# Kernel tuning notes

Measured on AMD Instinct MI355X. Metric: run time of the kernel, lower is better.

Reference implementation:

```python
import jax, jax.numpy as jnp
import numpy as np

VAR0, VAR1 = 0.1, 0.2   # cfg['variance']
THRESH = 0.5            # overlap_thresh
THETA = 0.01
NEGPOS = 3


def decode(loc, priors):
    # priors center-form [P,4]; returns point-form boxes [P,4]
    cxcy = priors[:, :2] + loc[:, :2] * VAR0 * priors[:, 2:]
    wh = priors[:, 2:] * jnp.exp(loc[:, 2:] * VAR1)
    return jnp.concatenate([cxcy - wh * 0.5, cxcy + wh * 0.5], axis=1)


def center_size(b):
    return jnp.concatenate([(b[:, :2] + b[:, 2:]) * 0.5, b[:, 2:] - b[:, :2]], axis=1)


def encode(matched, priors_c):
    # matched point-form [P,4], priors_c center-form [P,4]
    g_cxcy = ((matched[:, :2] + matched[:, 2:]) * 0.5 - priors_c[:, :2]) / (VAR0 * priors_c[:, 2:])
    g_wh = jnp.log((matched[:, 2:] - matched[:, :2]) / priors_c[:, 2:]) / VAR1
    return jnp.concatenate([g_cxcy, g_wh], axis=1)


def jaccard(a, b):
    # a [G,4], b [P,4] point form -> IoU [G,P]
    lt = jnp.maximum(a[:, None, :2], b[None, :, :2])
    rb = jnp.minimum(a[:, None, 2:], b[None, :, 2:])
    wh = jnp.clip(rb - lt, 0.0)
    inter = wh[..., 0] * wh[..., 1]
    area_a = ((a[:, 2] - a[:, 0]) * (a[:, 3] - a[:, 1]))[:, None]
    area_b = ((b[:, 2] - b[:, 0]) * (b[:, 3] - b[:, 1]))[None, :]
    return inter / (area_a + area_b - inter)


def _match_one(truths, labels, gt_mask, arm_loc, priors):
    # refine_match with arm_loc (use_ARM=True path)
    P = priors.shape[0]
    G = truths.shape[0]
    dec = decode(arm_loc, priors)                                 # [P,4]
    ov = jnp.where(gt_mask[:, None], jaccard(truths, dec), -1.0)  # [G,P], padded GT masked out
    best_prior_idx = jnp.argmax(ov, axis=1)                       # [G]
    best_truth_ov = jnp.max(ov, axis=0)                           # [P]
    best_truth_idx = jnp.argmax(ov, axis=0)                       # [P]
    safe = jnp.where(gt_mask, best_prior_idx, P)                  # OOB index -> dropped scatter
    best_truth_ov = best_truth_ov.at[safe].set(2.0, mode='drop')  # force-match each valid GT
    best_truth_idx = best_truth_idx.at[safe].set(jnp.arange(G), mode='drop')
    matched = truths[best_truth_idx]                              # [P,4]
    conf = jnp.where(best_truth_ov < THRESH, 0, labels[best_truth_idx])
    loc = encode(matched, center_size(dec))
    return loc, conf


def forward(arm_loc, arm_conf, odm_loc, odm_conf, priors, targets, num_gts):
    B, P, C = odm_conf.shape
    truths = targets[..., :4]
    labels = targets[..., 4].astype(jnp.int32)
    gt_mask = jnp.arange(targets.shape[1])[None, :] < num_gts[:, None]
    loc_t, conf_t = jax.vmap(_match_one, in_axes=(0, 0, 0, 0, None))(
        truths, labels, gt_mask,
        jax.lax.stop_gradient(arm_loc), jax.lax.stop_gradient(priors))
    loc_t = jax.lax.stop_gradient(loc_t)    # loc_t.requires_grad = False
    conf_t = jax.lax.stop_gradient(conf_t)

    # ARM objectness filter on positives
    p_obj = jax.nn.softmax(arm_conf, axis=2)[:, :, 1]
    pos = (conf_t > 0) & (p_obj > THETA)

    # masked smooth-L1 localization loss (sum)
    posf = pos[..., None].astype(odm_loc.dtype)
    d = jnp.abs(odm_loc * posf - loc_t * posf)
    loss_l = jnp.sum(jnp.where(d < 1.0, 0.5 * d * d, d - 0.5))

    # hard negative mining on per-prior softmax loss
    batch_conf = odm_conf.reshape(-1, C)
    lc = jax.nn.logsumexp(batch_conf, axis=1) - jnp.take_along_axis(
        batch_conf, conf_t.reshape(-1, 1), axis=1)[:, 0]
    lc = jnp.where(pos.reshape(-1), 0.0, lc).reshape(B, P)
    loss_idx = jnp.argsort(-lc, axis=1)
    idx_rank = jnp.argsort(loss_idx, axis=1)
    num_pos = jnp.sum(pos.astype(jnp.int32), axis=1, keepdims=True)  # [B,1]
    num_neg = jnp.minimum(NEGPOS * num_pos, P - 1)
    neg = idx_rank < num_neg
    mask = pos | neg

    # masked cross entropy (compute on zeroed-out logits like the original, then mask)
    conf_p = (odm_conf * mask[..., None].astype(odm_conf.dtype)).reshape(-1, C)
    tgt = jnp.where(mask, conf_t, 0).reshape(-1)
    logp = jax.nn.log_softmax(conf_p, axis=1)
    ce = -jnp.take_along_axis(logp, tgt[:, None], axis=1)[:, 0]
    loss_c = jnp.sum(ce * mask.reshape(-1).astype(ce.dtype))

    N = jnp.sum(num_pos).astype(jnp.float32)
    return loss_l / N, loss_c / N


def setup_inputs():
    key = jax.random.key(0)
    ks = jax.random.split(key, 10)
    B, P, C, G = 32, 16320, 21, 40
    arm_loc = jax.random.normal(ks[0], (B, P, 4), jnp.float32) * 0.1
    arm_conf = jax.random.normal(ks[1], (B, P, 2), jnp.float32)
    odm_loc = jax.random.normal(ks[2], (B, P, 4), jnp.float32) * 0.1
    odm_conf = jax.random.normal(ks[3], (B, P, C), jnp.float32)
    # priors in center form with positive sizes
    pc = jax.random.uniform(ks[4], (P, 2), jnp.float32, 0.1, 0.9)
    pwh = jax.random.uniform(ks[5], (P, 2), jnp.float32, 0.05, 0.3)
    priors = jnp.concatenate([pc, pwh], axis=1)
    # GT boxes in point form with positive area, labels in 1..C-1, padded to G=40
    gc = jax.random.uniform(ks[6], (B, G, 2), jnp.float32, 0.2, 0.8)
    gwh = jax.random.uniform(ks[7], (B, G, 2), jnp.float32, 0.05, 0.3)
    boxes = jnp.concatenate([gc - gwh * 0.5, gc + gwh * 0.5], axis=-1)
    labels = jax.random.randint(ks[8], (B, G, 1), 1, C).astype(jnp.float32)
    targets = jnp.concatenate([boxes, labels], axis=-1)
    num_gts = jax.random.randint(ks[9], (B,), 1, G + 1).astype(jnp.int32)
    return {"arm_loc": arm_loc, "arm_conf": arm_conf, "odm_loc": odm_loc,
            "odm_conf": odm_conf, "priors": priors, "targets": targets,
            "num_gts": num_gts}


def reference(arm_loc, arm_conf, odm_loc, odm_conf, priors, targets, num_gts):
    return forward(arm_loc, arm_conf, odm_loc, odm_conf, priors, targets, num_gts)
```

## Files before the change

### kernel.cpp

```cpp
#include <hip/hip_runtime.h>
#include <math.h>

#define VAR0 0.1f
#define VAR1 0.2f
#define THRESH 0.5f
#define THETA 0.01f
#define MAXG 64
#define BLK 256
#define SELT 1024
#define NCH 16
#define NB 4096
#define CAP 2048

__device__ __forceinline__ float4 decode_box(float4 l, float4 pr) {
    float cx = pr.x + l.x * VAR0 * pr.z;
    float cy = pr.y + l.y * VAR0 * pr.w;
    float w = pr.z * expf(l.z * VAR1);
    float h = pr.w * expf(l.w * VAR1);
    return make_float4(cx - w * 0.5f, cy - h * 0.5f, cx + w * 0.5f, cy + h * 0.5f);
}

__device__ __forceinline__ unsigned wave_umax_bits(unsigned v) {
    int x = (int)v;
    int t;
    t = __builtin_amdgcn_update_dpp(0, x, 0x111, 0xf, 0xf, true);  x = (t > x) ? t : x;
    t = __builtin_amdgcn_update_dpp(0, x, 0x112, 0xf, 0xf, true);  x = (t > x) ? t : x;
    t = __builtin_amdgcn_update_dpp(0, x, 0x114, 0xf, 0xf, true);  x = (t > x) ? t : x;
    t = __builtin_amdgcn_update_dpp(0, x, 0x118, 0xf, 0xf, true);  x = (t > x) ? t : x;
    t = __builtin_amdgcn_update_dpp(0, x, 0x142, 0xa, 0xf, false); x = (t > x) ? t : x;
    t = __builtin_amdgcn_update_dpp(0, x, 0x143, 0xc, 0xf, false); x = (t > x) ? t : x;
    return (unsigned)__builtin_amdgcn_readlane(x, 63);
}

__global__ void k_iou(const float* __restrict__ arm_loc, const float* __restrict__ priors,
                      const float* __restrict__ targets, const int* __restrict__ num_gts,
                      unsigned long long* __restrict__ bt,
                      unsigned long long* __restrict__ bpw,
                      int B, int P, int G) {
    int b = blockIdx.y;
    int p = blockIdx.x * blockDim.x + threadIdx.x;
    int tid = threadIdx.x;
    int lane = tid & 63, wid = tid >> 6;
    int wavebase = blockIdx.x * (int)blockDim.x + (tid & ~63);
    __shared__ float4 st4[MAXG];
    __shared__ float  stl[MAXG];
    __shared__ unsigned long long wk[4][MAXG];
    __shared__ int sng;
    if (tid == 0) sng = num_gts[b];
    for (int i = tid; i < G * 4; i += blockDim.x) {
        int g = i >> 2, k = i & 3;
        ((float*)&st4[g])[k] = targets[(size_t)b * G * 5 + g * 5 + k];
    }
    for (int g = tid; g < G; g += blockDim.x) stl[g] = targets[(size_t)b * G * 5 + g * 5 + 4];
    __syncthreads();
    int ng = sng;
    bool ok = p < P;
    float4 d = make_float4(0.f, 0.f, 0.f, 0.f);
    float areaB = 0.f;
    size_t i = (size_t)b * P + (ok ? p : 0);
    if (ok) {
        float4 l = ((const float4*)arm_loc)[i];
        float4 pr = ((const float4*)priors)[p];
        d = decode_box(l, pr);
        areaB = (d.z - d.x) * (d.w - d.y);
    }
    float bov = -2.0f; int bidx = 0;
    for (int g = 0; g < ng; ++g) {
        float4 t = st4[g];
        unsigned vbits = 0u;
        if (ok) {
            float lt0 = fmaxf(t.x, d.x), lt1 = fmaxf(t.y, d.y);
            float rb0 = fminf(t.z, d.z), rb1 = fminf(t.w, d.w);
            float w = rb0 - lt0; if (w < 0.f) w = 0.f;
            float h = rb1 - lt1; if (h < 0.f) h = 0.f;
            float inter = w * h;
            float areaA = (t.z - t.x) * (t.w - t.y);
            float ov = inter / (areaA + areaB - inter);
            if (ov > bov) { bov = ov; bidx = g; }
            vbits = __float_as_uint(ov);
        }
        unsigned om = wave_umax_bits(vbits);
        unsigned long long mask = __ballot(vbits == om);
        if (lane == 0) {
            int p_win = wavebase + (int)__builtin_ctzll(mask);
            wk[wid][g] = ((unsigned long long)om << 32)
                       | (unsigned long long)(0xFFFFFFFFu - (unsigned)p_win);
        }
    }
    if (ok)
        bt[i] = ((unsigned long long)__float_as_uint(bov) << 32) | (unsigned)bidx;
    __syncthreads();
    if (tid < ng) {
        unsigned long long k0 = wk[0][tid], k1 = wk[1][tid];
        unsigned long long k2 = wk[2][tid], k3 = wk[3][tid];
        unsigned long long m01 = k0 > k1 ? k0 : k1;
        unsigned long long m23 = k2 > k3 ? k2 : k3;
        unsigned long long m = m01 > m23 ? m01 : m23;
        bpw[(size_t)(b * G + tid) * gridDim.x + blockIdx.x] = m;
    }
}

__global__ void k_fix(const int* __restrict__ num_gts, const unsigned long long* __restrict__ bpw,
                      unsigned long long* __restrict__ bt, int B, int P, int G, int NBX) {
    int g = blockIdx.x, b = blockIdx.y;
    int lane = threadIdx.x;
    if (g >= num_gts[b]) return;
    const unsigned long long* src = bpw + (size_t)(b * G + g) * NBX;
    unsigned long long key = 0ull;
    for (int j = lane; j < NBX; j += 64) {
        unsigned long long v = src[j];
        if (v > key) key = v;
    }
    for (int off = 32; off > 0; off >>= 1) {
        unsigned long long o = __shfl_down(key, (unsigned)off, 64);
        if (o > key) key = o;
    }
    if (lane == 0) {
        unsigned p = 0xFFFFFFFFu - (unsigned)(key & 0xFFFFFFFFull);
        unsigned long long fkey = ((unsigned long long)0x40000000u << 32) | (unsigned)g;
        atomicMax(&bt[(size_t)b * P + p], fkey);
    }
}

__global__ void k_main(const float* __restrict__ arm_loc, const float* __restrict__ priors,
                       const float* __restrict__ arm_conf,
                       const float* __restrict__ odm_loc, const float* __restrict__ odm_conf,
                       const float* __restrict__ targets,
                       const unsigned long long* __restrict__ bt,
                       float* __restrict__ ce, unsigned char* __restrict__ posm,
                       float* __restrict__ partL, int* __restrict__ partN,
                       int B, int P, int C, int G) {
    int b = blockIdx.y;
    int p0 = blockIdx.x * BLK;
    int tid = threadIdx.x;
    int p = p0 + tid;
    __shared__ float4 st4[MAXG];
    __shared__ float  stl[MAXG];
    __shared__ float oc_s[BLK * 21];
    for (int i2 = tid; i2 < G * 4; i2 += BLK) {
        int g = i2 >> 2, k = i2 & 3;
        ((float*)&st4[g])[k] = targets[(size_t)b * G * 5 + g * 5 + k];
    }
    for (int g = tid; g < G; g += BLK) stl[g] = targets[(size_t)b * G * 5 + g * 5 + 4];
    int nrows = P - p0; if (nrows > BLK) nrows = BLK;
    int nf = nrows * C;
    const float* ocb = odm_conf + ((size_t)b * P + p0) * C;
    int nf4 = nf >> 2;
    const float4* ocb4 = (const float4*)ocb;
    for (int i2 = tid; i2 < nf4; i2 += BLK) ((float4*)oc_s)[i2] = ocb4[i2];
    if (tid < (nf & 3)) oc_s[(nf4 << 2) + tid] = ocb[(nf4 << 2) + tid];
    __syncthreads();
    float lsum = 0.f; int pc = 0;
    if (p < P) {
        size_t i = (size_t)b * P + p;
        unsigned long long mv = bt[i];
        float bov = __uint_as_float((unsigned)(mv >> 32));
        int bidx = (int)(mv & 0xFFFFFFFFull);
        int conf_t = (bov < THRESH) ? 0 : (int)stl[bidx];
        float2 c = ((const float2*)arm_conf)[i];
        float mm = fmaxf(c.x, c.y);
        float e0 = expf(c.x - mm), e1 = expf(c.y - mm);
        float p_obj = e1 / (e0 + e1);
        bool pos = (conf_t > 0) && (p_obj > THETA);
        if (pos) {
            pc = 1;
            float4 l = ((const float4*)arm_loc)[i];
            float4 pr = ((const float4*)priors)[p];
            float4 d = decode_box(l, pr);
            float pcx = (d.x + d.z) * 0.5f, pcy = (d.y + d.w) * 0.5f;
            float pw = d.z - d.x, ph = d.w - d.y;
            float4 t = st4[bidx];
            float g0 = ((t.x + t.z) * 0.5f - pcx) / (VAR0 * pw);
            float g1 = ((t.y + t.w) * 0.5f - pcy) / (VAR0 * ph);
            float g2 = logf((t.z - t.x) / pw) / VAR1;
            float g3 = logf((t.w - t.y) / ph) / VAR1;
            float4 ol = ((const float4*)odm_loc)[i];
            float dd;
            dd = fabsf(ol.x - g0); lsum += (dd < 1.f) ? 0.5f*dd*dd : dd - 0.5f;
            dd = fabsf(ol.y - g1); lsum += (dd < 1.f) ? 0.5f*dd*dd : dd - 0.5f;
            dd = fabsf(ol.z - g2); lsum += (dd < 1.f) ? 0.5f*dd*dd : dd - 0.5f;
            dd = fabsf(ol.w - g3); lsum += (dd < 1.f) ? 0.5f*dd*dd : dd - 0.5f;
        }
        const float* oc = oc_s + tid * C;
        float mx = oc[0];
        for (int j = 1; j < C; ++j) mx = fmaxf(mx, oc[j]);
        float sume = 0.f;
        for (int j = 0; j < C; ++j) sume += expf(oc[j] - mx);
        float lse = mx + logf(sume);
        float cev = lse - oc[conf_t];
        ce[i] = cev;
        posm[i] = pos ? 1 : 0;
    }
    __shared__ float rl[BLK];
    __shared__ int rc[BLK];
    rl[tid] = lsum; rc[tid] = pc;
    __syncthreads();
    for (int off = BLK/2; off > 0; off >>= 1) {
        if (tid < off) { rl[tid] += rl[tid+off]; rc[tid] += rc[tid+off]; }
        __syncthreads();
    }
    if (tid == 0) {
        partL[b * gridDim.x + blockIdx.x] = rl[0];
        partN[b * gridDim.x + blockIdx.x] = rc[0];
    }
}

__global__ __launch_bounds__(SELT) void k_select(
        const float* __restrict__ ce, const unsigned char* __restrict__ posm,
        const int* __restrict__ partN, int NBX,
        float* __restrict__ partC, int* __restrict__ npos, int P) {
    int b = blockIdx.x;
    int tid = threadIdx.x;
    int lane = tid & 63, wid = tid >> 6;
    __shared__ unsigned hist[NB];
    __shared__ float cv[CAP];
    __shared__ int   ci[CAP];
    __shared__ int   sums[SELT];
    __shared__ int   redi[16];
    __shared__ float redf[16];
    __shared__ int sh_base[16];
    __shared__ int sh_m, sh_b1, sh_k1, sh_npos, sh_istar, sh_kk, sh_cum;
    __shared__ unsigned sh_T, sh_pref;
    __shared__ float sh_mx;

    int c0 = 0;
    for (int j = tid; j < NBX; j += SELT) c0 += partN[b * NBX + j];
    for (int off = 32; off > 0; off >>= 1) c0 += __shfl_down(c0, (unsigned)off, 64);
    if (lane == 0) redi[wid] = c0;
    __syncthreads();
    if (tid < 64) {
        int v = (tid < 16) ? redi[tid] : 0;
        for (int off = 32; off > 0; off >>= 1) v += __shfl_down(v, (unsigned)off, 64);
        if (tid == 0) sh_npos = v;
    }
    __syncthreads();
    int npos_b = sh_npos;
    long K = 3L * npos_b;
    if (K > P - 1) K = P - 1;

    unsigned cb[NCH];
    unsigned lv[NCH];
    unsigned pmw = 0u;
    const unsigned* ceb = (const unsigned*)ce + (size_t)b * P;
    const unsigned char* pb = posm + (size_t)b * P;
    #pragma unroll
    for (int c = 0; c < NCH; ++c) {
        int i = c * SELT + tid;
        unsigned cbits = (i < P) ? ceb[i] : 0u;
        bool ps = (i < P) && (pb[i] != 0);
        cb[c] = cbits;
        if (ps) pmw |= (1u << c);
        lv[c] = ps ? 0u : cbits;
    }

    unsigned uT = 0xFFFFFFFFu; int istar = -1;
    if (K > 0) {
        float mx = 0.f;
        #pragma unroll
        for (int c = 0; c < NCH; ++c) mx = fmaxf(mx, __uint_as_float(lv[c]));
        for (int off = 32; off > 0; off >>= 1) mx = fmaxf(mx, __shfl_xor(mx, off, 64));
        if (lane == 0) redf[wid] = mx;
        __syncthreads();
        if (tid == 0) {
            float v = redf[0];
            for (int w = 1; w < 16; ++w) v = fmaxf(v, redf[w]);
            sh_mx = v;
        }
        __syncthreads();
        float vmax = sh_mx;
        float scale = (vmax > 0.f) ? ((float)NB / vmax) : 0.f;

        for (int j = tid; j < NB; j += SELT) hist[j] = 0u;
        __syncthreads();
        #pragma unroll
        for (int c = 0; c < NCH; ++c) {
            int i = c * SELT + tid;
            if (i < P) {
                int bn = (int)(__uint_as_float(lv[c]) * scale);
                if (bn > NB - 1) bn = NB - 1;
                atomicAdd(&hist[bn], 1u);
            }
        }
        __syncthreads();

        int s4 = (int)(hist[4*tid] + hist[4*tid+1] + hist[4*tid+2] + hist[4*tid+3]);
        sums[SELT - 1 - tid] = s4;
        __syncthreads();
        int x = sums[tid];
        int xs = x;
        for (int off = 1; off < 64; off <<= 1) {
            int o = __shfl_up(xs, (unsigned)off, 64);
            if (lane >= off) xs += o;
        }
        if (lane == 63) redi[wid] = xs;
        __syncthreads();
        if (tid < 64) {
            int v = (tid < 16) ? redi[tid] : 0;
            int vs = v;
            for (int off = 1; off < 16; off <<= 1) {
                int o = __shfl_up(vs, (unsigned)off, 64);
                if (lane >= off) vs += o;
            }
            if (tid < 16) redi[tid] = vs - v;
        }
        __syncthreads();
        int excl_rev = xs + redi[wid] - x;
        sums[tid] = excl_rev;
        __syncthreads();
        int suf = sums[SELT - 1 - tid];
        {
            int run = suf;
            for (int j = 3; j >= 0; --j) {
                int bin = 4 * tid + j;
                int h = (int)hist[bin];
                if ((long)run < K && K <= (long)run + h) { sh_b1 = bin; sh_k1 = (int)(K - run); }
                run += h;
            }
        }
        __syncthreads();
        int B1 = sh_b1, k1 = sh_k1;

        if (tid == 0) sh_m = 0;
        __syncthreads();
        #pragma unroll
        for (int c = 0; c < NCH; ++c) {
            int i = c * SELT + tid;
            if (i < P) {
                float f = __uint_as_float(lv[c]);
                int bn = (int)(f * scale);
                if (bn > NB - 1) bn = NB - 1;
                if (bn == B1) {
                    int pos = atomicAdd(&sh_m, 1);
                    if (pos < CAP) { cv[pos] = f; ci[pos] = i; }
                }
            }
        }
        __syncthreads();
        int m = sh_m;
        if (m <= CAP) {
            for (int j = tid; j < m; j += SELT) {
                float vj = cv[j]; int ij = ci[j]; int r = 0;
                for (int jj = 0; jj < m; ++jj) {
                    float vx = cv[jj];
                    r += (vx > vj || (vx == vj && ci[jj] < ij)) ? 1 : 0;
                }
                if (r == k1 - 1) { sh_T = __float_as_uint(vj); sh_istar = ij; }
            }
            __syncthreads();
            uT = sh_T; istar = sh_istar;
        } else {
            if (tid == 0) { sh_pref = 0u; sh_kk = (int)K; }
            __syncthreads();
            for (int bit = 30; bit >= 0; --bit) {
                unsigned pref = sh_pref;
                int kk = sh_kk;
                unsigned hi = pref >> (bit + 1);
                int cnt = 0;
                #pragma unroll
                for (int c = 0; c < NCH; ++c) {
                    int i = c * SELT + tid;
                    unsigned v = lv[c];
                    cnt += ((i < P) && ((v >> (bit + 1)) == hi) && ((v >> bit) & 1u)) ? 1 : 0;
                }
                for (int off = 32; off > 0; off >>= 1) cnt += __shfl_down(cnt, (unsigned)off, 64);
                if (lane == 0) redi[wid] = cnt;
                __syncthreads();
                if (tid < 64) {
                    int v = (tid < 16) ? redi[tid] : 0;
                    for (int off = 32; off > 0; off >>= 1) v += __shfl_down(v, (unsigned)off, 64);
                    if (tid == 0) {
                        if (kk <= v) sh_pref = pref | (1u << bit);
                        else sh_kk = kk - v;
                    }
                }
                __syncthreads();
            }
            unsigned T = sh_pref; int krem = sh_kk;
            if (tid == 0) { sh_istar = -1; sh_cum = 0; }
            __syncthreads();
            for (int c = 0; c < NCH; ++c) {
                int i = c * SELT + tid;
                bool eq = (i < P) && (lv[c] == T);
                unsigned long long mk = __ballot(eq);
                if (lane == 0) redi[wid] = (int)__popcll(mk);
                __syncthreads();
                if (tid < 64) {
                    int v = (tid < 16) ? redi[tid] : 0;
                    for (int off = 1; off < 16; off <<= 1) {
                        int o = __shfl_up(v, (unsigned)off, 64);
                        if (lane >= off) v += o;
                    }
                    if (tid < 16) sh_base[tid] = v;
                }
                __syncthreads();
                int cum = sh_cum;
                int base = (wid == 0) ? 0 : sh_base[wid - 1];
                if (eq) {
                    int r = cum + base + (int)__popcll(mk & ((1ull << lane) - 1ull));
                    if (r == krem - 1) sh_istar = i;
                }
                __syncthreads();
                if (tid == 0) sh_cum = cum + sh_base[15];
                __syncthreads();
                if (sh_cum >= krem) break;
            }
            __syncthreads();
            uT = T; istar = sh_istar;
        }
    }

    float cs = 0.f;
    #pragma unroll
    for (int c = 0; c < NCH; ++c) {
        int i = c * SELT + tid;
        if (i < P) {
            unsigned v = lv[c];
            bool sel = ((pmw >> c) & 1u) || (v > uT) || (v == uT && i <= istar);
            if (sel) cs += __uint_as_float(cb[c]);
        }
    }
    for (int off = 32; off > 0; off >>= 1) cs += __shfl_down(cs, (unsigned)off, 64);
    if (lane == 0) redf[wid] = cs;
    __syncthreads();
    if (tid < 64) {
        float v = (tid < 16) ? redf[tid] : 0.f;
        for (int off = 32; off > 0; off >>= 1) v += __shfl_down(v, (unsigned)off, 64);
        if (tid == 0) { partC[b] = v; npos[b] = npos_b; }
    }
}

__global__ void k_final(const float* __restrict__ partL, const float* __restrict__ partC,
                        const int* __restrict__ npos, int nPart,
                        float* __restrict__ out, int B) {
    __shared__ float sL[256];
    __shared__ float sC[256];
    __shared__ int   sN[256];
    int tid = threadIdx.x;
    float aL = 0.f, aC = 0.f; int aN = 0;
    for (int i = tid; i < nPart; i += 256) aL += partL[i];
    for (int i = tid; i < B; i += 256) { aC += partC[i]; aN += npos[i]; }
    sL[tid] = aL; sC[tid] = aC; sN[tid] = aN;
    __syncthreads();
    for (int off = 128; off > 0; off >>= 1) {
        if (tid < off) { sL[tid] += sL[tid+off]; sC[tid] += sC[tid+off]; sN[tid] += sN[tid+off]; }
        __syncthreads();
    }
    if (tid == 0) {
        float N = (float)sN[0];
        out[0] = sL[0] / N;
        out[1] = sC[0] / N;
    }
}

extern "C" void kernel_launch(void* const* d_in, const int* in_sizes, int n_in,
                              void* d_out, int out_size, void* d_ws, size_t ws_size,
                              hipStream_t stream) {
    const float* arm_loc  = (const float*)d_in[0];
    const float* arm_conf = (const float*)d_in[1];
    const float* odm_loc  = (const float*)d_in[2];
    const float* odm_conf = (const float*)d_in[3];
    const float* priors   = (const float*)d_in[4];
    const float* targets  = (const float*)d_in[5];
    const int*   num_gts  = (const int*)d_in[6];
    float* out = (float*)d_out;

    int B = in_sizes[6];
    int P = in_sizes[4] / 4;
    int C = in_sizes[3] / (B * P);
    int G = in_sizes[5] / (B * 5);
    int NBX = (P + BLK - 1) / BLK;

    char* ws = (char*)d_ws;
    size_t off = 0;
    auto alloc = [&](size_t bytes) -> void* {
        void* ptr = ws + off;
        off = (off + bytes + 255) & ~(size_t)255;
        return ptr;
    };
    unsigned long long* bt  = (unsigned long long*)alloc((size_t)B * P * 8);
    unsigned long long* bpw = (unsigned long long*)alloc((size_t)B * G * NBX * 8);
    float* ce  = (float*)alloc((size_t)B * P * sizeof(float));
    unsigned char* posm = (unsigned char*)alloc((size_t)B * P);
    float* partL = (float*)alloc((size_t)B * NBX * sizeof(float));
    int* partN   = (int*)alloc((size_t)B * NBX * sizeof(int));
    float* partC = (float*)alloc((size_t)B * sizeof(float));
    int* npos    = (int*)alloc((size_t)B * sizeof(int));

    k_iou<<<dim3(NBX, B), BLK, 0, stream>>>(arm_loc, priors, targets, num_gts, bt, bpw, B, P, G);
    k_fix<<<dim3(G, B), 64, 0, stream>>>(num_gts, bpw, bt, B, P, G, NBX);
    k_main<<<dim3(NBX, B), BLK, 0, stream>>>(arm_loc, priors, arm_conf, odm_loc, odm_conf, targets,
                                             bt, ce, posm, partL, partN, B, P, C, G);
    k_select<<<B, SELT, 0, stream>>>(ce, posm, partN, NBX, partC, npos, P);
    k_final<<<1, 256, 0, stream>>>(partL, partC, npos, B * NBX, out, B);
}
```

Baseline: 64.12 us.

## Fuse IoU matching with loss kernel and patch forced matches afterwards

Merges the IoU/argmax kernel and the per-prior loss kernel into one pass, so the best-truth result no longer makes a round trip through global memory. Forced best-prior matches are then applied as a per-batch delta patch that corrects ce, posm, the positive count and the localization loss for the affected priors. Per-batch loss totals move into k_select, and k_final shrinks to a single-wave reduction. This removes one kernel launch and the bt buffer, but packs bidx into the low bits of the overlap float and adds delta-correction logic that must handle duplicate forced priors correctly.

```diff
diff --git a/kernel.cpp b/kernel.cpp
--- a/kernel.cpp
+++ b/kernel.cpp
@@ -20,6 +20,21 @@
     return make_float4(cx - w * 0.5f, cy - h * 0.5f, cx + w * 0.5f, cy + h * 0.5f);
 }
 
+__device__ __forceinline__ float smooth_l1_sum(float4 ol, float4 t, float4 d) {
+    float pcx = (d.x + d.z) * 0.5f, pcy = (d.y + d.w) * 0.5f;
+    float pw = d.z - d.x, ph = d.w - d.y;
+    float g0 = ((t.x + t.z) * 0.5f - pcx) / (VAR0 * pw);
+    float g1 = ((t.y + t.w) * 0.5f - pcy) / (VAR0 * ph);
+    float g2 = logf((t.z - t.x) / pw) / VAR1;
+    float g3 = logf((t.w - t.y) / ph) / VAR1;
+    float s = 0.f, dd;
+    dd = fabsf(ol.x - g0); s += (dd < 1.f) ? 0.5f*dd*dd : dd - 0.5f;
+    dd = fabsf(ol.y - g1); s += (dd < 1.f) ? 0.5f*dd*dd : dd - 0.5f;
+    dd = fabsf(ol.z - g2); s += (dd < 1.f) ? 0.5f*dd*dd : dd - 0.5f;
+    dd = fabsf(ol.w - g3); s += (dd < 1.f) ? 0.5f*dd*dd : dd - 0.5f;
+    return s;
+}
+
 __device__ __forceinline__ unsigned wave_umax_bits(unsigned v) {
     int x = (int)v;
     int t;
@@ -32,26 +47,42 @@
     return (unsigned)__builtin_amdgcn_readlane(x, 63);
 }
 
-__global__ void k_iou(const float* __restrict__ arm_loc, const float* __restrict__ priors,
-                      const float* __restrict__ targets, const int* __restrict__ num_gts,
-                      unsigned long long* __restrict__ bt,
-                      unsigned long long* __restrict__ bpw,
-                      int B, int P, int G) {
+__global__ void k_fused(const float* __restrict__ arm_loc, const float* __restrict__ priors,
+                        const float* __restrict__ arm_conf,
+                        const float* __restrict__ odm_loc, const float* __restrict__ odm_conf,
+                        const float* __restrict__ targets, const int* __restrict__ num_gts,
+                        float* __restrict__ ce, unsigned char* __restrict__ posm,
+                        unsigned* __restrict__ bb,
+                        unsigned long long* __restrict__ bpw,
+                        float* __restrict__ partL, int* __restrict__ partN,
+                        int B, int P, int C, int G) {
     int b = blockIdx.y;
-    int p = blockIdx.x * blockDim.x + threadIdx.x;
+    int p0 = blockIdx.x * BLK;
     int tid = threadIdx.x;
+    int p = p0 + tid;
     int lane = tid & 63, wid = tid >> 6;
-    int wavebase = blockIdx.x * (int)blockDim.x + (tid & ~63);
+    int wavebase = p0 + (tid & ~63);
     __shared__ float4 st4[MAXG];
     __shared__ float  stl[MAXG];
+    __shared__ float  sarea[MAXG];
     __shared__ unsigned long long wk[4][MAXG];
+    __shared__ float oc_s[BLK * 21];
     __shared__ int sng;
     if (tid == 0) sng = num_gts[b];
-    for (int i = tid; i < G * 4; i += blockDim.x) {
-        int g = i >> 2, k = i & 3;
-        ((float*)&st4[g])[k] = targets[(size_t)b * G * 5 + g * 5 + k];
-    }
-    for (int g = tid; g < G; g += blockDim.x) stl[g] = targets[(size_t)b * G * 5 + g * 5 + 4];
+    for (int g = tid; g < G; g += BLK) {
+        const float* tg = targets + (size_t)b * G * 5 + g * 5;
+        float t0 = tg[0], t1 = tg[1], t2 = tg[2], t3 = tg[3];
+        st4[g] = make_float4(t0, t1, t2, t3);
+        stl[g] = tg[4];
+        sarea[g] = (t2 - t0) * (t3 - t1);
+    }
+    int nrows = P - p0; if (nrows > BLK) nrows = BLK;
+    int nf = nrows * C;
+    const float* ocb = odm_conf + ((size_t)b * P + p0) * C;
+    int nf4 = nf >> 2;
+    const float4* ocb4 = (const float4*)ocb;
+    for (int i2 = tid; i2 < nf4; i2 += BLK) ((float4*)oc_s)[i2] = ocb4[i2];
+    if (tid < (nf & 3)) oc_s[(nf4 << 2) + tid] = ocb[(nf4 << 2) + tid];
     __syncthreads();
     int ng = sng;
     bool ok = p < P;
@@ -74,88 +105,24 @@
             float w = rb0 - lt0; if (w < 0.f) w = 0.f;
             float h = rb1 - lt1; if (h < 0.f) h = 0.f;
             float inter = w * h;
-            float areaA = (t.z - t.x) * (t.w - t.y);
-            float ov = inter / (areaA + areaB - inter);
+            float ov = inter / (sarea[g] + areaB - inter);
             if (ov > bov) { bov = ov; bidx = g; }
             vbits = __float_as_uint(ov);
         }
         unsigned om = wave_umax_bits(vbits);
-        unsigned long long mask = __ballot(vbits == om);
+        unsigned long long mask = __ballot(ok && vbits == om);
         if (lane == 0) {
-            int p_win = wavebase + (int)__builtin_ctzll(mask);
-            wk[wid][g] = ((unsigned long long)om << 32)
-                       | (unsigned long long)(0xFFFFFFFFu - (unsigned)p_win);
-        }
-    }
-    if (ok)
-        bt[i] = ((unsigned long long)__float_as_uint(bov) << 32) | (unsigned)bidx;
-    __syncthreads();
-    if (tid < ng) {
-        unsigned long long k0 = wk[0][tid], k1 = wk[1][tid];
-        unsigned long long k2 = wk[2][tid], k3 = wk[3][tid];
-        unsigned long long m01 = k0 > k1 ? k0 : k1;
-        unsigned long long m23 = k2 > k3 ? k2 : k3;
-        unsigned long long m = m01 > m23 ? m01 : m23;
-        bpw[(size_t)(b * G + tid) * gridDim.x + blockIdx.x] = m;
-    }
-}
-
-__global__ void k_fix(const int* __restrict__ num_gts, const unsigned long long* __restrict__ bpw,
-                      unsigned long long* __restrict__ bt, int B, int P, int G, int NBX) {
-    int g = blockIdx.x, b = blockIdx.y;
-    int lane = threadIdx.x;
-    if (g >= num_gts[b]) return;
-    const unsigned long long* src = bpw + (size_t)(b * G + g) * NBX;
-    unsigned long long key = 0ull;
-    for (int j = lane; j < NBX; j += 64) {
-        unsigned long long v = src[j];
-        if (v > key) key = v;
-    }
-    for (int off = 32; off > 0; off >>= 1) {
-        unsigned long long o = __shfl_down(key, (unsigned)off, 64);
-        if (o > key) key = o;
-    }
-    if (lane == 0) {
-        unsigned p = 0xFFFFFFFFu - (unsigned)(key & 0xFFFFFFFFull);
-        unsigned long long fkey = ((unsigned long long)0x40000000u << 32) | (unsigned)g;
-        atomicMax(&bt[(size_t)b * P + p], fkey);
-    }
-}
-
-__global__ void k_main(const float* __restrict__ arm_loc, const float* __restrict__ priors,
-                       const float* __restrict__ arm_conf,
-                       const float* __restrict__ odm_loc, const float* __restrict__ odm_conf,
-                       const float* __restrict__ targets,
-                       const unsigned long long* __restrict__ bt,
-                       float* __restrict__ ce, unsigned char* __restrict__ posm,
-                       float* __restrict__ partL, int* __restrict__ partN,
-                       int B, int P, int C, int G) {
-    int b = blockIdx.y;
-    int p0 = blockIdx.x * BLK;
-    int tid = threadIdx.x;
-    int p = p0 + tid;
-    __shared__ float4 st4[MAXG];
-    __shared__ float  stl[MAXG];
-    __shared__ float oc_s[BLK * 21];
-    for (int i2 = tid; i2 < G * 4; i2 += BLK) {
-        int g = i2 >> 2, k = i2 & 3;
-        ((float*)&st4[g])[k] = targets[(size_t)b * G * 5 + g * 5 + k];
-    }
-    for (int g = tid; g < G; g += BLK) stl[g] = targets[(size_t)b * G * 5 + g * 5 + 4];
-    int nrows = P - p0; if (nrows > BLK) nrows = BLK;
-    int nf = nrows * C;
-    const float* ocb = odm_conf + ((size_t)b * P + p0) * C;
-    int nf4 = nf >> 2;
-    const float4* ocb4 = (const float4*)ocb;
-    for (int i2 = tid; i2 < nf4; i2 += BLK) ((float4*)oc_s)[i2] = ocb4[i2];
-    if (tid < (nf & 3)) oc_s[(nf4 << 2) + tid] = ocb[(nf4 << 2) + tid];
-    __syncthreads();
+            unsigned long long key = 0ull;
+            if (mask) {
+                int p_win = wavebase + (int)__builtin_ctzll(mask);
+                key = ((unsigned long long)om << 32)
+                    | (unsigned long long)(0xFFFFFFFFu - (unsigned)p_win);
+            }
+            wk[wid][g] = key;
+        }
+    }
     float lsum = 0.f; int pc = 0;
-    if (p < P) {
-        size_t i = (size_t)b * P + p;
-        unsigned long long mv = bt[i];
-        float bov = __uint_as_float((unsigned)(mv >> 32));
-        int bidx = (int)(mv & 0xFFFFFFFFull);
+    if (ok) {
         int conf_t = (bov < THRESH) ? 0 : (int)stl[bidx];
         float2 c = ((const float2*)arm_conf)[i];
         float mm = fmaxf(c.x, c.y);
@@ -164,22 +131,8 @@
         bool pos = (conf_t > 0) && (p_obj > THETA);
         if (pos) {
             pc = 1;
-            float4 l = ((const float4*)arm_loc)[i];
-            float4 pr = ((const float4*)priors)[p];
-            float4 d = decode_box(l, pr);
-            float pcx = (d.x + d.z) * 0.5f, pcy = (d.y + d.w) * 0.5f;
-            float pw = d.z - d.x, ph = d.w - d.y;
-            float4 t = st4[bidx];
-            float g0 = ((t.x + t.z) * 0.5f - pcx) / (VAR0 * pw);
-            float g1 = ((t.y + t.w) * 0.5f - pcy) / (VAR0 * ph);
-            float g2 = logf((t.z - t.x) / pw) / VAR1;
-            float g3 = logf((t.w - t.y) / ph) / VAR1;
             float4 ol = ((const float4*)odm_loc)[i];
-            float dd;
-            dd = fabsf(ol.x - g0); lsum += (dd < 1.f) ? 0.5f*dd*dd : dd - 0.5f;
-            dd = fabsf(ol.y - g1); lsum += (dd < 1.f) ? 0.5f*dd*dd : dd - 0.5f;
-            dd = fabsf(ol.z - g2); lsum += (dd < 1.f) ? 0.5f*dd*dd : dd - 0.5f;
-            dd = fabsf(ol.w - g3); lsum += (dd < 1.f) ? 0.5f*dd*dd : dd - 0.5f;
+            lsum = smooth_l1_sum(ol, st4[bidx], d);
         }
         const float* oc = oc_s + tid * C;
         float mx = oc[0];
@@ -190,11 +143,20 @@
         float cev = lse - oc[conf_t];
         ce[i] = cev;
         posm[i] = pos ? 1 : 0;
+        bb[i] = (__float_as_uint(bov) & 0xFFFFFFC0u) | (unsigned)bidx;
     }
     __shared__ float rl[BLK];
     __shared__ int rc[BLK];
     rl[tid] = lsum; rc[tid] = pc;
     __syncthreads();
+    if (tid < ng) {
+        unsigned long long k0 = wk[0][tid], k1 = wk[1][tid];
+        unsigned long long k2 = wk[2][tid], k3 = wk[3][tid];
+        unsigned long long m01 = k0 > k1 ? k0 : k1;
+        unsigned long long m23 = k2 > k3 ? k2 : k3;
+        unsigned long long m = m01 > m23 ? m01 : m23;
+        bpw[(size_t)(b * G + tid) * gridDim.x + blockIdx.x] = m;
+    }
     for (int off = BLK/2; off > 0; off >>= 1) {
         if (tid < off) { rl[tid] += rl[tid+off]; rc[tid] += rc[tid+off]; }
         __syncthreads();
@@ -205,10 +167,93 @@
     }
 }
 
+__global__ __launch_bounds__(1024) void k_fixpatch(
+        const float* __restrict__ arm_loc, const float* __restrict__ priors,
+        const float* __restrict__ arm_conf, const float* __restrict__ odm_loc,
+        const float* __restrict__ odm_conf,
+        const float* __restrict__ targets, const int* __restrict__ num_gts,
+        const unsigned long long* __restrict__ bpw, const unsigned* __restrict__ bb,
+        float* __restrict__ ce, unsigned char* __restrict__ posm,
+        float* __restrict__ partPL, int* __restrict__ partPN,
+        int B, int P, int C, int G, int NBX) {
+    int b = blockIdx.x;
+    int tid = threadIdx.x;
+    int lane = tid & 63, wid = tid >> 6;
+    __shared__ int fp[MAXG];
+    __shared__ float4 st4[MAXG];
+    __shared__ float  stl[MAXG];
+    __shared__ int sng;
+    if (tid == 0) sng = num_gts[b];
+    for (int g = tid; g < G; g += 1024) {
+        const float* tg = targets + (size_t)b * G * 5 + g * 5;
+        st4[g] = make_float4(tg[0], tg[1], tg[2], tg[3]);
+        stl[g] = tg[4];
+    }
+    __syncthreads();
+    int ng = sng;
+    for (int g = wid; g < ng; g += 16) {
+        const unsigned long long* src = bpw + (size_t)(b * G + g) * NBX;
+        unsigned long long key = 0ull;
+        for (int j = lane; j < NBX; j += 64) {
+            unsigned long long v = src[j];
+            if (v > key) key = v;
+        }
+        for (int off = 32; off > 0; off >>= 1) {
+            unsigned long long o = __shfl_down(key, (unsigned)off, 64);
+            if (o > key) key = o;
+        }
+        if (lane == 0) fp[g] = (int)(0xFFFFFFFFu - (unsigned)(key & 0xFFFFFFFFull));
+    }
+    __syncthreads();
+    if (tid < G) {
+        float dL = 0.f; int dN = 0;
+        if (tid < ng) {
+            int g = tid;
+            bool dup = false;
+            for (int g2 = g + 1; g2 < ng; ++g2) if (fp[g2] == fp[g]) { dup = true; break; }
+            if (!dup) {
+                int p = fp[g];
+                size_t i = (size_t)b * P + p;
+                unsigned bbv = bb[i];
+                int old_bidx = (int)(bbv & 63u);
+                bool old_ge = __uint_as_float(bbv & 0xFFFFFFC0u) >= THRESH;
+                int old_ct = old_ge ? (int)stl[old_bidx] : 0;
+                int new_ct = (int)stl[g];
+                float2 c = ((const float2*)arm_conf)[i];
+                float mm = fmaxf(c.x, c.y);
+                float e0 = expf(c.x - mm), e1 = expf(c.y - mm);
+                float p_obj = e1 / (e0 + e1);
+                bool old_pos = (old_ct > 0) && (p_obj > THETA);
+                bool new_pos = (p_obj > THETA);
+                if (old_pos || new_pos) {
+                    float4 l = ((const float4*)arm_loc)[i];
+                    float4 pr = ((const float4*)priors)[p];
+                    float4 d = decode_box(l, pr);
+                    float4 ol = ((const float4*)odm_loc)[i];
+                    if (old_pos) dL -= smooth_l1_sum(ol, st4[old_bidx], d);
+                    if (new_pos) dL += smooth_l1_sum(ol, st4[g], d);
+                }
+                dN = (new_pos ? 1 : 0) - (old_pos ? 1 : 0);
+                const float* oc = odm_conf + i * (size_t)C;
+                float ce_old = ce[i];
+                float ce_new = (old_ct == new_ct) ? ce_old
+                             : (ce_old + oc[old_ct] - oc[new_ct]);
+                ce[i] = ce_new;
+                posm[i] = new_pos ? 1 : 0;
+            }
+        }
+        partPL[b * G + tid] = dL;
+        partPN[b * G + tid] = dN;
+    }
+}
+
 __global__ __launch_bounds__(SELT) void k_select(
         const float* __restrict__ ce, const unsigned char* __restrict__ posm,
-        const int* __restrict__ partN, int NBX,
-        float* __restrict__ partC, int* __restrict__ npos, int P) {
+        const int* __restrict__ partN, const int* __restrict__ partPN,
+        const float* __restrict__ partL, const float* __restrict__ partPL,
+        int NBX, int G,
+        float* __restrict__ partC, float* __restrict__ totL,
+        int* __restrict__ npos, int P) {
     int b = blockIdx.x;
     int tid = threadIdx.x;
     int lane = tid & 63, wid = tid >> 6;
@@ -221,17 +266,25 @@
     __shared__ int sh_base[16];
     __shared__ int sh_m, sh_b1, sh_k1, sh_npos, sh_istar, sh_kk, sh_cum;
     __shared__ unsigned sh_T, sh_pref;
-    __shared__ float sh_mx;
-
-    int c0 = 0;
-    for (int j = tid; j < NBX; j += SELT) c0 += partN[b * NBX + j];
-    for (int off = 32; off > 0; off >>= 1) c0 += __shfl_down(c0, (unsigned)off, 64);
-    if (lane == 0) redi[wid] = c0;
+    __shared__ float sh_mx, sh_totl;
+
+    int c0 = 0; float l0 = 0.f;
+    for (int j = tid; j < NBX; j += SELT) { c0 += partN[b * NBX + j]; l0 += partL[b * NBX + j]; }
+    for (int g = tid; g < G; g += SELT)   { c0 += partPN[b * G + g];  l0 += partPL[b * G + g]; }
+    for (int off = 32; off > 0; off >>= 1) {
+        c0 += __shfl_down(c0, (unsigned)off, 64);
+        l0 += __shfl_down(l0, (unsigned)off, 64);
+    }
+    if (lane == 0) { redi[wid] = c0; redf[wid] = l0; }
     __syncthreads();
     if (tid < 64) {
         int v = (tid < 16) ? redi[tid] : 0;
-        for (int off = 32; off > 0; off >>= 1) v += __shfl_down(v, (unsigned)off, 64);
-        if (tid == 0) sh_npos = v;
+        float f = (tid < 16) ? redf[tid] : 0.f;
+        for (int off = 32; off > 0; off >>= 1) {
+            v += __shfl_down(v, (unsigned)off, 64);
+            f += __shfl_down(f, (unsigned)off, 64);
+        }
+        if (tid == 0) { sh_npos = v; sh_totl = f; }
     }
     __syncthreads();
     int npos_b = sh_npos;
@@ -425,30 +478,25 @@
     if (tid < 64) {
         float v = (tid < 16) ? redf[tid] : 0.f;
         for (int off = 32; off > 0; off >>= 1) v += __shfl_down(v, (unsigned)off, 64);
-        if (tid == 0) { partC[b] = v; npos[b] = npos_b; }
-    }
-}
-
-__global__ void k_final(const float* __restrict__ partL, const float* __restrict__ partC,
-                        const int* __restrict__ npos, int nPart,
-                        float* __restrict__ out, int B) {
-    __shared__ float sL[256];
-    __shared__ float sC[256];
-    __shared__ int   sN[256];
+        if (tid == 0) { partC[b] = v; npos[b] = npos_b; totL[b] = sh_totl; }
+    }
+}
+
+__global__ void k_final(const float* __restrict__ totL, const float* __restrict__ partC,
+                        const int* __restrict__ npos, float* __restrict__ out, int B) {
     int tid = threadIdx.x;
-    float aL = 0.f, aC = 0.f; int aN = 0;
-    for (int i = tid; i < nPart; i += 256) aL += partL[i];
-    for (int i = tid; i < B; i += 256) { aC += partC[i]; aN += npos[i]; }
-    sL[tid] = aL; sC[tid] = aC; sN[tid] = aN;
-    __syncthreads();
-    for (int off = 128; off > 0; off >>= 1) {
-        if (tid < off) { sL[tid] += sL[tid+off]; sC[tid] += sC[tid+off]; sN[tid] += sN[tid+off]; }
-        __syncthreads();
+    float aL = (tid < B) ? totL[tid] : 0.f;
+    float aC = (tid < B) ? partC[tid] : 0.f;
+    int   aN = (tid < B) ? npos[tid] : 0;
+    for (int off = 32; off > 0; off >>= 1) {
+        aL += __shfl_down(aL, (unsigned)off, 64);
+        aC += __shfl_down(aC, (unsigned)off, 64);
+        aN += __shfl_down(aN, (unsigned)off, 64);
     }
     if (tid == 0) {
-        float N = (float)sN[0];
-        out[0] = sL[0] / N;
-        out[1] = sC[0] / N;
+        float N = (float)aN;
+        out[0] = aL / N;
+        out[1] = aC / N;
     }
 }
 
@@ -477,19 +525,25 @@
         off = (off + bytes + 255) & ~(size_t)255;
         return ptr;
     };
-    unsigned long long* bt  = (unsigned long long*)alloc((size_t)B * P * 8);
     unsigned long long* bpw = (unsigned long long*)alloc((size_t)B * G * NBX * 8);
+    unsigned* bb = (unsigned*)alloc((size_t)B * P * 4);
     float* ce  = (float*)alloc((size_t)B * P * sizeof(float));
     unsigned char* posm = (unsigned char*)alloc((size_t)B * P);
     float* partL = (float*)alloc((size_t)B * NBX * sizeof(float));
     int* partN   = (int*)alloc((size_t)B * NBX * sizeof(int));
+    float* partPL = (float*)alloc((size_t)B * G * sizeof(float));
+    int* partPN   = (int*)alloc((size_t)B * G * sizeof(int));
     float* partC = (float*)alloc((size_t)B * sizeof(float));
+    float* totL  = (float*)alloc((size_t)B * sizeof(float));
     int* npos    = (int*)alloc((size_t)B * sizeof(int));
 
-    k_iou<<<dim3(NBX, B), BLK, 0, stream>>>(arm_loc, priors, targets, num_gts, bt, bpw, B, P, G);
-    k_fix<<<dim3(G, B), 64, 0, stream>>>(num_gts, bpw, bt, B, P, G, NBX);
-    k_main<<<dim3(NBX, B), BLK, 0, stream>>>(arm_loc, priors, arm_conf, odm_loc, odm_conf, targets,
-                                             bt, ce, posm, partL, partN, B, P, C, G);
-    k_select<<<B, SELT, 0, stream>>>(ce, posm, partN, NBX, partC, npos, P);
-    k_final<<<1, 256, 0, stream>>>(partL, partC, npos, B * NBX, out, B);
-}
+    k_fused<<<dim3(NBX, B), BLK, 0, stream>>>(arm_loc, priors, arm_conf, odm_loc, odm_conf,
+                                              targets, num_gts, ce, posm, bb, bpw,
+                                              partL, partN, B, P, C, G);
+    k_fixpatch<<<B, 1024, 0, stream>>>(arm_loc, priors, arm_conf, odm_loc, odm_conf,
+                                       targets, num_gts, bpw, bb, ce, posm,
+                                       partPL, partPN, B, P, C, G, NBX);
+    k_select<<<B, SELT, 0, stream>>>(ce, posm, partN, partPN, partL, partPL,
+                                     NBX, G, partC, totL, npos, P);
+    k_final<<<1, 64, 0, stream>>>(totL, partC, npos, out, B);
+}
```

Result: slower. 65.73 us (+2.5%).
